# Optimization experiments

Measured on AMD Instinct MI355X. Metric: run time of the kernel, lower is better.

The kernel has to match this reference:

```python
import jax, jax.numpy as jnp
import numpy as np

D, NP, NC, ITERS = 2048, 64, 32, 3
B, L = 4, 4096
EPS = 1e-6


def setup_inputs() -> dict:
    key = jax.random.key(0)
    ks = jax.random.split(key, 10)
    sc = lambda k, shape, s: (jax.random.normal(k, shape, jnp.float32) * s)
    return {
        "x": jax.random.normal(ks[0], (B, L, D), jnp.float32),
        "prop_w": sc(ks[1], (NP, D), 0.02),
        "prop_b": jnp.zeros((NP,), jnp.float32),
        "constraint_mat": sc(ks[2], (NC, NP), 0.1),
        "polarity": sc(ks[3], (NC, NP), 0.1),
        "corr_w1": sc(ks[4], (2 * NP, 2 * NP), 0.08),
        "corr_b1": jnp.zeros((2 * NP,), jnp.float32),
        "corr_w2": sc(ks[5], (NP, 2 * NP), 0.08),
        "corr_b2": jnp.zeros((NP,), jnp.float32),
        "cons_w": sc(ks[6], (1, NC), 0.1),
        "cons_b": jnp.zeros((1,), jnp.float32),
        "emb_w": sc(ks[7], (D, NP), 0.02),
        "emb_b": jnp.zeros((D,), jnp.float32),
        "norm_w": jnp.ones((D,), jnp.float32),
    }


def reference(x, prop_w, prop_b, constraint_mat, polarity,
              corr_w1, corr_b1, corr_w2, corr_b2,
              cons_w, cons_b, emb_w, emb_b, norm_w):
    n_p = prop_w.shape[0]
    n_c = constraint_mat.shape[0]
    W = jax.nn.sigmoid(constraint_mat)  # [n_c, n_p] constraint strength
    P = jax.nn.sigmoid(polarity)        # [n_c, n_p] polarity

    def check(props):
        # mean_j(W_ij*p_j + P_ij*(1-p_j)) == (p @ W.T + (1-p) @ P.T) / n_p
        return (props @ W.T + (1.0 - props) @ P.T) / n_p  # [B,L,n_c]

    props = jax.nn.sigmoid(x @ prop_w.T + prop_b)  # [B,L,n_p]
    for _ in range(ITERS):
        violation = 1.0 - check(props)                 # [B,L,n_c]
        viol_signal = (violation @ W) / (n_c + 1e-06)  # [B,L,n_p]
        h = jnp.concatenate([props, viol_signal], axis=-1)  # [B,L,2*n_p]
        h = jax.nn.gelu(h @ corr_w1.T + corr_b1, approximate=False)
        props = jax.nn.sigmoid(h @ corr_w2.T + corr_b2)

    satisfaction = check(props)                              # [B,L,n_c]
    consistency = jax.nn.sigmoid(satisfaction @ cons_w.T + cons_b)  # [B,L,1]
    violation_loss = jnp.mean(1.0 - satisfaction)
    symbolic = props @ emb_w.T + emb_b                       # [B,L,D]
    y = x + symbolic * consistency
    y = y * jax.lax.rsqrt(jnp.mean(y * y, axis=-1, keepdims=True) + EPS) * norm_w
    return (y, props, satisfaction, consistency, violation_loss)
```

## Files before the change

### kernel.cpp

```cpp
#include <hip/hip_runtime.h>
#include <hip/hip_bf16.h>
#include <cstdint>

#define D     2048
#define NP    64
#define NC    32
#define T     16384

#define Y_OFF   0
#define P_OFF   33554432
#define S_OFF   34603008
#define C_OFF   35127296
#define L_OFF   35143680

#define WS_LPART 0
#define WS_SUMP  1024
#define WS_PWF   1056
#define WS_EF    66592
#define WS_W1F   132128
#define WS_W2F   140320
#define WS_WMF   144416
#define WS_WLF   145440

typedef short short8 __attribute__((ext_vector_type(8)));
typedef float f32x4 __attribute__((ext_vector_type(4)));

__device__ __forceinline__ float sigf(float z) { return 1.0f / (1.0f + __expf(-z)); }
__device__ __forceinline__ short f2bf(float f) {
  unsigned u = __float_as_uint(f);
  return (short)((u + 0x8000u) >> 16);
}
__device__ __forceinline__ unsigned pk2(float a, float b) {
  return ((unsigned)(unsigned short)f2bf(a)) | (((unsigned)(unsigned short)f2bf(b)) << 16);
}

__global__ __launch_bounds__(256) void k0_prep(const float* __restrict__ cm, const float* __restrict__ pol,
                                               const float* __restrict__ w1, const float* __restrict__ w2,
                                               const float* __restrict__ pw, const float* __restrict__ ew,
                                               float* __restrict__ ws) {
  int gid = blockIdx.x * 256 + threadIdx.x;
  int stride = gridDim.x * 256;
  short* pwF = (short*)(ws + WS_PWF);
  for (int idx = gid; idx < 64 * 4 * 64; idx += stride) {
    int kc = idx >> 8, jt = (idx >> 6) & 3, l = idx & 63;
    int j = 16 * jt + (l & 15), k = 32 * kc + 8 * (l >> 4);
    const float* src = &pw[(size_t)j * D + k];
    short8 v;
#pragma unroll
    for (int e = 0; e < 8; ++e) v[e] = f2bf(src[e]);
    *(short8*)&pwF[idx * 8] = v;
  }
  short* eF = (short*)(ws + WS_EF);
  for (int idx = gid; idx < 128 * 2 * 64; idx += stride) {
    int dt = idx >> 7, kc = (idx >> 6) & 1, l = idx & 63;
    int d = 16 * dt + (l & 15), j = 32 * kc + 8 * (l >> 4);
    const float* src = &ew[(size_t)d * NP + j];
    short8 v;
#pragma unroll
    for (int e = 0; e < 8; ++e) v[e] = f2bf(src[e]);
    *(short8*)&eF[idx * 8] = v;
  }
  short* w1F = (short*)(ws + WS_W1F);
  for (int idx = gid; idx < 8 * 4 * 64; idx += stride) {
    int nt = idx >> 8, kc = (idx >> 6) & 3, l = idx & 63;
    int m = 16 * nt + (l & 15), k = 32 * kc + 8 * (l >> 4);
    const float* src = &w1[(size_t)m * 128 + k];
    short8 v;
#pragma unroll
    for (int e = 0; e < 8; ++e) v[e] = f2bf(src[e]);
    *(short8*)&w1F[idx * 8] = v;
  }
  short* w2F = (short*)(ws + WS_W2F);
  for (int idx = gid; idx < 4 * 4 * 64; idx += stride) {
    int nt = idx >> 8, kc = (idx >> 6) & 3, l = idx & 63;
    int j = 16 * nt + (l & 15), k = 32 * kc + 8 * (l >> 4);
    const float* src = &w2[(size_t)j * 128 + k];
    short8 v;
#pragma unroll
    for (int e = 0; e < 8; ++e) v[e] = f2bf(src[e]);
    *(short8*)&w2F[idx * 8] = v;
  }
  short* wmF = (short*)(ws + WS_WMF);
  for (int idx = gid; idx < 2 * 2 * 64; idx += stride) {
    int nt = idx >> 7, kc = (idx >> 6) & 1, l = idx & 63;
    int i = 16 * nt + (l & 15), j = 32 * kc + 8 * (l >> 4);
    short8 v;
#pragma unroll
    for (int e = 0; e < 8; ++e)
      v[e] = f2bf(sigf(cm[i * 64 + j + e]) - sigf(pol[i * 64 + j + e]));
    *(short8*)&wmF[idx * 8] = v;
  }
  short* wlF = (short*)(ws + WS_WLF);
  for (int idx = gid; idx < 4 * 64; idx += stride) {
    int nt = idx >> 6, l = idx & 63;
    int j = 16 * nt + (l & 15), i0 = 8 * (l >> 4);
    short8 v;
#pragma unroll
    for (int e = 0; e < 8; ++e) v[e] = f2bf(sigf(cm[(i0 + e) * 64 + j]));
    *(short8*)&wlF[idx * 8] = v;
  }
  if (gid < NC) {
    float s = 0.f;
    for (int j = 0; j < NP; ++j) s += sigf(pol[gid * NP + j]);
    ws[WS_SUMP + gid] = s;
  }
}

__global__ __launch_bounds__(256) void k1_props(const float* __restrict__ x, const float* __restrict__ ws,
                                                const float* __restrict__ pb, float* __restrict__ props0) {
  __shared__ char XT[8192];
  int tid = threadIdx.x, lane = tid & 63;
  int jt = __builtin_amdgcn_readfirstlane(tid >> 6);
  int wv = tid >> 6;
  int t0 = blockIdx.x * 16;
  int lr = lane & 15, lg = lane >> 4;
  int c64 = tid & 63;
  const short* pwF = (const short*)(ws + WS_PWF);

  f32x4 acc = {0.f, 0.f, 0.f, 0.f};
  for (int c = 0; c < 8; ++c) {
    float4 st[4];
#pragma unroll
    for (int j = 0; j < 4; ++j)
      st[j] = *(const float4*)&x[(size_t)(t0 + wv + 4 * j) * D + 256 * c + 4 * c64];
    __syncthreads();
#pragma unroll
    for (int j = 0; j < 4; ++j) {
      int tt = wv + 4 * j;
      int off = (tt * 512 + 8 * c64) ^ ((tt & 7) << 4);
      uint2 p = make_uint2(pk2(st[j].x, st[j].y), pk2(st[j].z, st[j].w));
      *(uint2*)(XT + off) = p;
    }
    __syncthreads();
#pragma unroll
    for (int kcL = 0; kcL < 8; ++kcL) {
      const short8 b = *(const short8*)(XT + ((lr * 512 + 64 * kcL + 16 * lg) ^ ((lr & 7) << 4)));
      const short8 a = *(const short8*)&pwF[(((8 * c + kcL) * 4 + jt) * 64 + lane) * 8];
      acc = __builtin_amdgcn_mfma_f32_16x16x32_bf16(a, b, acc, 0, 0, 0);
    }
  }
  int j0 = 16 * jt + 4 * lg;
  const float4 pbv = *(const float4*)&pb[j0];
  float4 o;
  o.x = sigf(acc[0] + pbv.x); o.y = sigf(acc[1] + pbv.y);
  o.z = sigf(acc[2] + pbv.z); o.w = sigf(acc[3] + pbv.w);
  *(float4*)&props0[(size_t)(t0 + lr) * 64 + j0] = o;
}

__global__ __launch_bounds__(64) void k2_iter(const float* __restrict__ ws,
                                              const float* __restrict__ b1, const float* __restrict__ b2,
                                              const float* __restrict__ cw, const float* __restrict__ cb,
                                              const float* __restrict__ props0, float* __restrict__ out,
                                              float* __restrict__ lpart) {
  __shared__ char Lraw[9216];
  char* Hb = Lraw;
  char* H2b = Lraw + 4096;
  char* SBb = Lraw + 8192;
  int lane = threadIdx.x & 63;
  int lr = lane & 15, lg = lane >> 4;
  int t0 = blockIdx.x * 16;
  const short8* w1F = (const short8*)(ws + WS_W1F);
  const short8* w2F = (const short8*)(ws + WS_W2F);
  const short8* wmF = (const short8*)(ws + WS_WMF);
  const short8* wlF = (const short8*)(ws + WS_WLF);
  const float* SUMP = ws + WS_SUMP;

  float b1v[8], b2v[4], sumpv[2], cwv[2];
#pragma unroll
  for (int nt = 0; nt < 8; ++nt) b1v[nt] = b1[16 * nt + lr];
#pragma unroll
  for (int nt = 0; nt < 4; ++nt) b2v[nt] = b2[16 * nt + lr];
#pragma unroll
  for (int nt = 0; nt < 2; ++nt) { sumpv[nt] = SUMP[16 * nt + lr]; cwv[nt] = cw[16 * nt + lr]; }
  float cb0 = cb[0];

#pragma unroll
  for (int r = 0; r < 4; ++r) {
    int idx = r * 64 + lane;
    int t = idx >> 4, c4 = idx & 15;
    const float4 v = *(const float4*)&props0[(size_t)(t0 + t) * 64 + 4 * c4];
    int off = (t * 256 + c4 * 8) ^ ((t & 7) << 4);
    *(unsigned*)(Hb + off) = pk2(v.x, v.y);
    *(unsigned*)(Hb + off + 4) = pk2(v.z, v.w);
  }
  __syncthreads();

  const f32x4 zf = {0.f, 0.f, 0.f, 0.f};
  f32x4 s0, s1;

#define LDF(base, row, kelem, rowB) \
  (*(const short8*)((base) + ((((row) * (rowB)) + (kelem) * 2) ^ (((row) & 7) << 4))))
#define STBF(base, row, kelem, rowB, val) \
  (*(short*)((base) + ((((row) * (rowB)) + (kelem) * 2) ^ (((row) & 7) << 4))) = f2bf(val))

  for (int it = 0; it < 3; ++it) {
    short8 ap0 = LDF(Hb, lr, 8 * lg, 256);
    short8 ap1 = LDF(Hb, lr, 32 + 8 * lg, 256);
    s0 = zf; s1 = zf;
    s0 = __builtin_amdgcn_mfma_f32_16x16x32_bf16(ap0, wmF[0 * 64 + lane], s0, 0, 0, 0);
    s0 = __builtin_amdgcn_mfma_f32_16x16x32_bf16(ap1, wmF[1 * 64 + lane], s0, 0, 0, 0);
    s1 = __builtin_amdgcn_mfma_f32_16x16x32_bf16(ap0, wmF[2 * 64 + lane], s1, 0, 0, 0);
    s1 = __builtin_amdgcn_mfma_f32_16x16x32_bf16(ap1, wmF[3 * 64 + lane], s1, 0, 0, 0);
#pragma unroll
    for (int q = 0; q < 4; ++q) {
      int t = 4 * lg + q;
      STBF(SBb, t, lr, 64, 1.f - (s0[q] + sumpv[0]) * (1.f / 64.f));
      STBF(SBb, t, 16 + lr, 64, 1.f - (s1[q] + sumpv[1]) * (1.f / 64.f));
    }
    __syncthreads();

    short8 as = LDF(SBb, lr, 8 * lg, 64);
    f32x4 vv0 = __builtin_amdgcn_mfma_f32_16x16x32_bf16(as, wlF[0 * 64 + lane], zf, 0, 0, 0);
    f32x4 vv1 = __builtin_amdgcn_mfma_f32_16x16x32_bf16(as, wlF[1 * 64 + lane], zf, 0, 0, 0);
    f32x4 vv2 = __builtin_amdgcn_mfma_f32_16x16x32_bf16(as, wlF[2 * 64 + lane], zf, 0, 0, 0);
    f32x4 vv3 = __builtin_amdgcn_mfma_f32_16x16x32_bf16(as, wlF[3 * 64 + lane], zf, 0, 0, 0);
    const float vs = 1.0f / (32.0f + 1e-6f);
#pragma unroll
    for (int q = 0; q < 4; ++q) {
      int t = 4 * lg + q;
      STBF(Hb, t, 64 + lr, 256, vv0[q] * vs);
      STBF(Hb, t, 64 + 16 + lr, 256, vv1[q] * vs);
      STBF(Hb, t, 64 + 32 + lr, 256, vv2[q] * vs);
      STBF(Hb, t, 64 + 48 + lr, 256, vv3[q] * vs);
    }
    __syncthreads();

    short8 ah2 = LDF(Hb, lr, 64 + 8 * lg, 256);
    short8 ah3 = LDF(Hb, lr, 96 + 8 * lg, 256);
    f32x4 g1[8];
#pragma unroll
    for (int nt = 0; nt < 8; ++nt) {
      f32x4 a = zf;
      a = __builtin_amdgcn_mfma_f32_16x16x32_bf16(ap0, w1F[(nt * 4 + 0) * 64 + lane], a, 0, 0, 0);
      a = __builtin_amdgcn_mfma_f32_16x16x32_bf16(ap1, w1F[(nt * 4 + 1) * 64 + lane], a, 0, 0, 0);
      a = __builtin_amdgcn_mfma_f32_16x16x32_bf16(ah2, w1F[(nt * 4 + 2) * 64 + lane], a, 0, 0, 0);
      a = __builtin_amdgcn_mfma_f32_16x16x32_bf16(ah3, w1F[(nt * 4 + 3) * 64 + lane], a, 0, 0, 0);
      g1[nt] = a;
    }
#pragma unroll
    for (int nt = 0; nt < 8; ++nt) {
#pragma unroll
      for (int q = 0; q < 4; ++q) {
        float v = g1[nt][q] + b1v[nt];
        float gl = 0.5f * v * (1.0f + erff(v * 0.70710678118654752f));
        STBF(H2b, 4 * lg + q, 16 * nt + lr, 256, gl);
      }
    }
    __syncthreads();

    short8 ab0 = LDF(H2b, lr, 8 * lg, 256);
    short8 ab1 = LDF(H2b, lr, 32 + 8 * lg, 256);
    short8 ab2 = LDF(H2b, lr, 64 + 8 * lg, 256);
    short8 ab3 = LDF(H2b, lr, 96 + 8 * lg, 256);
#pragma unroll
    for (int nt = 0; nt < 4; ++nt) {
      f32x4 a = zf;
      a = __builtin_amdgcn_mfma_f32_16x16x32_bf16(ab0, w2F[(nt * 4 + 0) * 64 + lane], a, 0, 0, 0);
      a = __builtin_amdgcn_mfma_f32_16x16x32_bf16(ab1, w2F[(nt * 4 + 1) * 64 + lane], a, 0, 0, 0);
      a = __builtin_amdgcn_mfma_f32_16x16x32_bf16(ab2, w2F[(nt * 4 + 2) * 64 + lane], a, 0, 0, 0);
      a = __builtin_amdgcn_mfma_f32_16x16x32_bf16(ab3, w2F[(nt * 4 + 3) * 64 + lane], a, 0, 0, 0);
#pragma unroll
      for (int q = 0; q < 4; ++q) {
        int t = 4 * lg + q;
        float p = sigf(a[q] + b2v[nt]);
        STBF(Hb, t, 16 * nt + lr, 256, p);
        if (it == 2) out[P_OFF + (size_t)(t0 + t) * 64 + 16 * nt + lr] = p;
      }
    }
    __syncthreads();
  }

  {
    short8 ap0 = LDF(Hb, lr, 8 * lg, 256);
    short8 ap1 = LDF(Hb, lr, 32 + 8 * lg, 256);
    s0 = zf; s1 = zf;
    s0 = __builtin_amdgcn_mfma_f32_16x16x32_bf16(ap0, wmF[0 * 64 + lane], s0, 0, 0, 0);
    s0 = __builtin_amdgcn_mfma_f32_16x16x32_bf16(ap1, wmF[1 * 64 + lane], s0, 0, 0, 0);
    s1 = __builtin_amdgcn_mfma_f32_16x16x32_bf16(ap0, wmF[2 * 64 + lane], s1, 0, 0, 0);
    s1 = __builtin_amdgcn_mfma_f32_16x16x32_bf16(ap1, wmF[3 * 64 + lane], s1, 0, 0, 0);
    float ls = 0.f;
    float csum[4];
#pragma unroll
    for (int q = 0; q < 4; ++q) {
      int t = 4 * lg + q;
      float sa = (s0[q] + sumpv[0]) * (1.f / 64.f);
      float sb = (s1[q] + sumpv[1]) * (1.f / 64.f);
      out[S_OFF + (size_t)(t0 + t) * 32 + lr] = sa;
      out[S_OFF + (size_t)(t0 + t) * 32 + 16 + lr] = sb;
      ls += (1.f - sa) + (1.f - sb);
      csum[q] = cwv[0] * sa + cwv[1] * sb;
    }
#pragma unroll
    for (int m = 1; m <= 8; m <<= 1) {
#pragma unroll
      for (int q = 0; q < 4; ++q) csum[q] += __shfl_xor(csum[q], m);
    }
    if (lr == 0) {
#pragma unroll
      for (int q = 0; q < 4; ++q)
        out[C_OFF + t0 + 4 * lg + q] = sigf(csum[q] + cb0);
    }
#pragma unroll
    for (int m = 1; m <= 32; m <<= 1) ls += __shfl_xor(ls, m);
    if (lane == 0) lpart[blockIdx.x] = ls;
  }
#undef LDF
#undef STBF
}

__global__ __launch_bounds__(512) void k3n(const float* __restrict__ x, const float* __restrict__ ws,
                                           const float* __restrict__ eb, const float* __restrict__ nw,
                                           float* __restrict__ out) {
  __shared__ float ssp[8][16];
  __shared__ float sc16[16];
  int tid = threadIdx.x, lane = tid & 63;
  int wu = __builtin_amdgcn_readfirstlane(tid >> 6);
  int t0 = blockIdx.x * 16;
  int lr = lane & 15, lg = lane >> 4;
  const short* eF = (const short*)(ws + WS_EF);

  const float* pr = out + P_OFF + (size_t)(t0 + lr) * 64 + 8 * lg;
  const float4 q0 = *(const float4*)pr;
  const float4 q1 = *(const float4*)(pr + 4);
  const float4 q2 = *(const float4*)(pr + 32);
  const float4 q3 = *(const float4*)(pr + 36);
  short8 p0, p1;
  p0[0] = f2bf(q0.x); p0[1] = f2bf(q0.y); p0[2] = f2bf(q0.z); p0[3] = f2bf(q0.w);
  p0[4] = f2bf(q1.x); p0[5] = f2bf(q1.y); p0[6] = f2bf(q1.z); p0[7] = f2bf(q1.w);
  p1[0] = f2bf(q2.x); p1[1] = f2bf(q2.y); p1[2] = f2bf(q2.z); p1[3] = f2bf(q2.w);
  p1[4] = f2bf(q3.x); p1[5] = f2bf(q3.y); p1[6] = f2bf(q3.z); p1[7] = f2bf(q3.w);

  float consv = out[C_OFF + t0 + lr];

  f32x4 yv[16];
  float ss = 0.f;
#pragma unroll
  for (int dt2 = 0; dt2 < 16; ++dt2) {
    int dt = wu * 16 + dt2;
    const short8 e0 = *(const short8*)&eF[((dt * 2 + 0) * 64 + lane) * 8];
    const short8 e1 = *(const short8*)&eF[((dt * 2 + 1) * 64 + lane) * 8];
    f32x4 acc = {0.f, 0.f, 0.f, 0.f};
    acc = __builtin_amdgcn_mfma_f32_16x16x32_bf16(e0, p0, acc, 0, 0, 0);
    acc = __builtin_amdgcn_mfma_f32_16x16x32_bf16(e1, p1, acc, 0, 0, 0);
    int d0 = 16 * dt + 4 * lg;
    const float4 ebv = *(const float4*)&eb[d0];
    const float4 xv = *(const float4*)&x[(size_t)(t0 + lr) * D + d0];
    f32x4 y;
    y[0] = fmaf(acc[0] + ebv.x, consv, xv.x);
    y[1] = fmaf(acc[1] + ebv.y, consv, xv.y);
    y[2] = fmaf(acc[2] + ebv.z, consv, xv.z);
    y[3] = fmaf(acc[3] + ebv.w, consv, xv.w);
    ss += y[0] * y[0] + y[1] * y[1] + y[2] * y[2] + y[3] * y[3];
    yv[dt2] = y;
  }
  ss += __shfl_xor(ss, 16);
  ss += __shfl_xor(ss, 32);
  if (lg == 0) ssp[wu][lr] = ss;
  __syncthreads();
  if (tid < 16) {
    float s = 0.f;
#pragma unroll
    for (int w = 0; w < 8; ++w) s += ssp[w][tid];
    sc16[tid] = rsqrtf(s * (1.0f / 2048.0f) + 1e-6f);
  }
  __syncthreads();
  float sc = sc16[lr];
#pragma unroll
  for (int dt2 = 0; dt2 < 16; ++dt2) {
    int d0 = 16 * (wu * 16 + dt2) + 4 * lg;
    const float4 nwv = *(const float4*)&nw[d0];
    float4 o;
    o.x = yv[dt2][0] * sc * nwv.x;
    o.y = yv[dt2][1] * sc * nwv.y;
    o.z = yv[dt2][2] * sc * nwv.z;
    o.w = yv[dt2][3] * sc * nwv.w;
    *(float4*)&out[Y_OFF + (size_t)(t0 + lr) * D + d0] = o;
  }
}

__global__ __launch_bounds__(256) void k4_loss(const float* __restrict__ lpart, float* __restrict__ loss) {
  __shared__ float w[4];
  int tid = threadIdx.x;
  float v = 0.f;
#pragma unroll
  for (int r = 0; r < 4; ++r) v += lpart[tid + 256 * r];
  for (int o = 32; o > 0; o >>= 1) v += __shfl_down(v, o);
  if ((tid & 63) == 0) w[tid >> 6] = v;
  __syncthreads();
  if (tid == 0)
    loss[0] = (w[0] + w[1] + w[2] + w[3]) * (1.0f / (16384.0f * 32.0f));
}

extern "C" void kernel_launch(void* const* d_in, const int* in_sizes, int n_in,
                              void* d_out, int out_size, void* d_ws, size_t ws_size,
                              hipStream_t stream) {
  (void)in_sizes; (void)n_in; (void)out_size; (void)ws_size;
  const float* x   = (const float*)d_in[0];
  const float* pw  = (const float*)d_in[1];
  const float* pb  = (const float*)d_in[2];
  const float* cm  = (const float*)d_in[3];
  const float* pol = (const float*)d_in[4];
  const float* w1  = (const float*)d_in[5];
  const float* b1  = (const float*)d_in[6];
  const float* w2  = (const float*)d_in[7];
  const float* b2  = (const float*)d_in[8];
  const float* cw  = (const float*)d_in[9];
  const float* cb  = (const float*)d_in[10];
  const float* ew  = (const float*)d_in[11];
  const float* eb  = (const float*)d_in[12];
  const float* nw  = (const float*)d_in[13];
  float* out = (float*)d_out;
  float* ws  = (float*)d_ws;

  hipLaunchKernelGGL(k0_prep, dim3(64), dim3(256), 0, stream, cm, pol, w1, w2, pw, ew, ws);
  hipLaunchKernelGGL(k1_props, dim3(1024), dim3(256), 0, stream, x, ws, pb, out + Y_OFF);
  hipLaunchKernelGGL(k2_iter, dim3(1024), dim3(64), 0, stream, ws, b1, b2, cw, cb,
                     out + Y_OFF, out, ws + WS_LPART);
  hipLaunchKernelGGL(k4_loss, dim3(1), dim3(256), 0, stream, ws + WS_LPART, out + L_OFF);
  hipLaunchKernelGGL(k3n, dim3(1024), dim3(512), 0, stream, x, ws, eb, nw, out);
}
```

Baseline: 128.9 us.

## Fuse props projection with refinement, double-buffer x tiles, fold loss into norm

Merges the property projection and the iterative refinement into one kernel. The sigmoid props now go straight into LDS as bf16 instead of taking a global round trip, and one fewer launch is needed. The x tile load is double-buffered so global loads overlap the MFMA work. Inside the single-wave refinement, block barriers become LDS waitcnt fences. The separate loss-reduction kernel is folded into one wave of the final norm kernel. The norm kernel also holds y in bf16 registers to save VGPRs, which costs some output precision before the RMS scaling.

```diff
diff --git a/kernel.cpp b/kernel.cpp
--- a/kernel.cpp
+++ b/kernel.cpp
@@ -106,9 +106,15 @@
   }
 }
 
-__global__ __launch_bounds__(256) void k1_props(const float* __restrict__ x, const float* __restrict__ ws,
-                                                const float* __restrict__ pb, float* __restrict__ props0) {
-  __shared__ char XT[8192];
+__global__ __launch_bounds__(256, 4) void k12(const float* __restrict__ x, const float* __restrict__ ws,
+                                              const float* __restrict__ pb,
+                                              const float* __restrict__ b1, const float* __restrict__ b2,
+                                              const float* __restrict__ cw, const float* __restrict__ cb,
+                                              float* __restrict__ out, float* __restrict__ lpart) {
+  __shared__ __align__(16) char L[20480];
+  char* Hb = L;
+  char* H2b = L + 4096;
+  char* SBb = L + 8192;
   int tid = threadIdx.x, lane = tid & 63;
   int jt = __builtin_amdgcn_readfirstlane(tid >> 6);
   int wv = tid >> 6;
@@ -118,47 +124,54 @@
   const short* pwF = (const short*)(ws + WS_PWF);
 
   f32x4 acc = {0.f, 0.f, 0.f, 0.f};
-  for (int c = 0; c < 8; ++c) {
+  {
     float4 st[4];
 #pragma unroll
     for (int j = 0; j < 4; ++j)
-      st[j] = *(const float4*)&x[(size_t)(t0 + wv + 4 * j) * D + 256 * c + 4 * c64];
-    __syncthreads();
+      st[j] = *(const float4*)&x[(size_t)(t0 + wv + 4 * j) * D + 4 * c64];
+    char* XTw = L + 4096;
 #pragma unroll
     for (int j = 0; j < 4; ++j) {
       int tt = wv + 4 * j;
       int off = (tt * 512 + 8 * c64) ^ ((tt & 7) << 4);
-      uint2 p = make_uint2(pk2(st[j].x, st[j].y), pk2(st[j].z, st[j].w));
-      *(uint2*)(XT + off) = p;
-    }
-    __syncthreads();
-#pragma unroll
-    for (int kcL = 0; kcL < 8; ++kcL) {
-      const short8 b = *(const short8*)(XT + ((lr * 512 + 64 * kcL + 16 * lg) ^ ((lr & 7) << 4)));
-      const short8 a = *(const short8*)&pwF[(((8 * c + kcL) * 4 + jt) * 64 + lane) * 8];
-      acc = __builtin_amdgcn_mfma_f32_16x16x32_bf16(a, b, acc, 0, 0, 0);
-    }
-  }
-  int j0 = 16 * jt + 4 * lg;
-  const float4 pbv = *(const float4*)&pb[j0];
-  float4 o;
-  o.x = sigf(acc[0] + pbv.x); o.y = sigf(acc[1] + pbv.y);
-  o.z = sigf(acc[2] + pbv.z); o.w = sigf(acc[3] + pbv.w);
-  *(float4*)&props0[(size_t)(t0 + lr) * 64 + j0] = o;
-}
-
-__global__ __launch_bounds__(64) void k2_iter(const float* __restrict__ ws,
-                                              const float* __restrict__ b1, const float* __restrict__ b2,
-                                              const float* __restrict__ cw, const float* __restrict__ cb,
-                                              const float* __restrict__ props0, float* __restrict__ out,
-                                              float* __restrict__ lpart) {
-  __shared__ char Lraw[9216];
-  char* Hb = Lraw;
-  char* H2b = Lraw + 4096;
-  char* SBb = Lraw + 8192;
-  int lane = threadIdx.x & 63;
-  int lr = lane & 15, lg = lane >> 4;
-  int t0 = blockIdx.x * 16;
+      *(uint2*)(XTw + off) = make_uint2(pk2(st[j].x, st[j].y), pk2(st[j].z, st[j].w));
+    }
+    for (int c = 0; c < 8; ++c) {
+      if (c < 7) {
+#pragma unroll
+        for (int j = 0; j < 4; ++j)
+          st[j] = *(const float4*)&x[(size_t)(t0 + wv + 4 * j) * D + 256 * (c + 1) + 4 * c64];
+      }
+      __syncthreads();
+      const char* XTr = L + 4096 + (c & 1) * 8192;
+#pragma unroll
+      for (int kcL = 0; kcL < 8; ++kcL) {
+        const short8 b = *(const short8*)(XTr + ((lr * 512 + 64 * kcL + 16 * lg) ^ ((lr & 7) << 4)));
+        const short8 a = *(const short8*)&pwF[(((8 * c + kcL) * 4 + jt) * 64 + lane) * 8];
+        acc = __builtin_amdgcn_mfma_f32_16x16x32_bf16(a, b, acc, 0, 0, 0);
+      }
+      if (c < 7) {
+        char* XTn = L + 4096 + ((c + 1) & 1) * 8192;
+#pragma unroll
+        for (int j = 0; j < 4; ++j) {
+          int tt = wv + 4 * j;
+          int off = (tt * 512 + 8 * c64) ^ ((tt & 7) << 4);
+          *(uint2*)(XTn + off) = make_uint2(pk2(st[j].x, st[j].y), pk2(st[j].z, st[j].w));
+        }
+      }
+    }
+  }
+  {
+    int j0 = 16 * jt + 4 * lg;
+    const float4 pbv = *(const float4*)&pb[j0];
+    float p0 = sigf(acc[0] + pbv.x), p1 = sigf(acc[1] + pbv.y);
+    float p2 = sigf(acc[2] + pbv.z), p3 = sigf(acc[3] + pbv.w);
+    int off = (lr * 256 + j0 * 2) ^ ((lr & 7) << 4);
+    *(uint2*)(Hb + off) = make_uint2(pk2(p0, p1), pk2(p2, p3));
+  }
+  __syncthreads();
+  if (wv != 0) return;
+
   const short8* w1F = (const short8*)(ws + WS_W1F);
   const short8* w2F = (const short8*)(ws + WS_W2F);
   const short8* wmF = (const short8*)(ws + WS_WMF);
@@ -174,20 +187,10 @@
   for (int nt = 0; nt < 2; ++nt) { sumpv[nt] = SUMP[16 * nt + lr]; cwv[nt] = cw[16 * nt + lr]; }
   float cb0 = cb[0];
 
-#pragma unroll
-  for (int r = 0; r < 4; ++r) {
-    int idx = r * 64 + lane;
-    int t = idx >> 4, c4 = idx & 15;
-    const float4 v = *(const float4*)&props0[(size_t)(t0 + t) * 64 + 4 * c4];
-    int off = (t * 256 + c4 * 8) ^ ((t & 7) << 4);
-    *(unsigned*)(Hb + off) = pk2(v.x, v.y);
-    *(unsigned*)(Hb + off + 4) = pk2(v.z, v.w);
-  }
-  __syncthreads();
-
   const f32x4 zf = {0.f, 0.f, 0.f, 0.f};
   f32x4 s0, s1;
 
+#define LDSFENCE asm volatile("s_waitcnt lgkmcnt(0)" ::: "memory")
 #define LDF(base, row, kelem, rowB) \
   (*(const short8*)((base) + ((((row) * (rowB)) + (kelem) * 2) ^ (((row) & 7) << 4))))
 #define STBF(base, row, kelem, rowB, val) \
@@ -207,7 +210,7 @@
       STBF(SBb, t, lr, 64, 1.f - (s0[q] + sumpv[0]) * (1.f / 64.f));
       STBF(SBb, t, 16 + lr, 64, 1.f - (s1[q] + sumpv[1]) * (1.f / 64.f));
     }
-    __syncthreads();
+    LDSFENCE;
 
     short8 as = LDF(SBb, lr, 8 * lg, 64);
     f32x4 vv0 = __builtin_amdgcn_mfma_f32_16x16x32_bf16(as, wlF[0 * 64 + lane], zf, 0, 0, 0);
@@ -223,7 +226,7 @@
       STBF(Hb, t, 64 + 32 + lr, 256, vv2[q] * vs);
       STBF(Hb, t, 64 + 48 + lr, 256, vv3[q] * vs);
     }
-    __syncthreads();
+    LDSFENCE;
 
     short8 ah2 = LDF(Hb, lr, 64 + 8 * lg, 256);
     short8 ah3 = LDF(Hb, lr, 96 + 8 * lg, 256);
@@ -246,7 +249,7 @@
         STBF(H2b, 4 * lg + q, 16 * nt + lr, 256, gl);
       }
     }
-    __syncthreads();
+    LDSFENCE;
 
     short8 ab0 = LDF(H2b, lr, 8 * lg, 256);
     short8 ab1 = LDF(H2b, lr, 32 + 8 * lg, 256);
@@ -267,7 +270,7 @@
         if (it == 2) out[P_OFF + (size_t)(t0 + t) * 64 + 16 * nt + lr] = p;
       }
     }
-    __syncthreads();
+    LDSFENCE;
   }
 
   {
@@ -306,11 +309,12 @@
   }
 #undef LDF
 #undef STBF
-}
-
-__global__ __launch_bounds__(512) void k3n(const float* __restrict__ x, const float* __restrict__ ws,
-                                           const float* __restrict__ eb, const float* __restrict__ nw,
-                                           float* __restrict__ out) {
+#undef LDSFENCE
+}
+
+__global__ __launch_bounds__(512, 4) void k3n(const float* __restrict__ x, const float* __restrict__ ws,
+                                              const float* __restrict__ eb, const float* __restrict__ nw,
+                                              const float* __restrict__ lpart, float* __restrict__ out) {
   __shared__ float ssp[8][16];
   __shared__ float sc16[16];
   int tid = threadIdx.x, lane = tid & 63;
@@ -318,6 +322,15 @@
   int t0 = blockIdx.x * 16;
   int lr = lane & 15, lg = lane >> 4;
   const short* eF = (const short*)(ws + WS_EF);
+
+  if (blockIdx.x == 0 && wu == 7) {
+    float v = 0.f;
+#pragma unroll
+    for (int r = 0; r < 16; ++r) v += lpart[lane + 64 * r];
+#pragma unroll
+    for (int m = 1; m <= 32; m <<= 1) v += __shfl_xor(v, m);
+    if (lane == 0) out[L_OFF] = v * (1.0f / (16384.0f * 32.0f));
+  }
 
   const float* pr = out + P_OFF + (size_t)(t0 + lr) * 64 + 8 * lg;
   const float4 q0 = *(const float4*)pr;
@@ -332,9 +345,9 @@
 
   float consv = out[C_OFF + t0 + lr];
 
-  f32x4 yv[16];
+  uint2 yv[16];
   float ss = 0.f;
-#pragma unroll
+#pragma unroll 4
   for (int dt2 = 0; dt2 < 16; ++dt2) {
     int dt = wu * 16 + dt2;
     const short8 e0 = *(const short8*)&eF[((dt * 2 + 0) * 64 + lane) * 8];
@@ -345,13 +358,12 @@
     int d0 = 16 * dt + 4 * lg;
     const float4 ebv = *(const float4*)&eb[d0];
     const float4 xv = *(const float4*)&x[(size_t)(t0 + lr) * D + d0];
-    f32x4 y;
-    y[0] = fmaf(acc[0] + ebv.x, consv, xv.x);
-    y[1] = fmaf(acc[1] + ebv.y, consv, xv.y);
-    y[2] = fmaf(acc[2] + ebv.z, consv, xv.z);
-    y[3] = fmaf(acc[3] + ebv.w, consv, xv.w);
-    ss += y[0] * y[0] + y[1] * y[1] + y[2] * y[2] + y[3] * y[3];
-    yv[dt2] = y;
+    float y0 = fmaf(acc[0] + ebv.x, consv, xv.x);
+    float y1 = fmaf(acc[1] + ebv.y, consv, xv.y);
+    float y2 = fmaf(acc[2] + ebv.z, consv, xv.z);
+    float y3 = fmaf(acc[3] + ebv.w, consv, xv.w);
+    ss += y0 * y0 + y1 * y1 + y2 * y2 + y3 * y3;
+    yv[dt2] = make_uint2(pk2(y0, y1), pk2(y2, y3));
   }
   ss += __shfl_xor(ss, 16);
   ss += __shfl_xor(ss, 32);
@@ -365,30 +377,18 @@
   }
   __syncthreads();
   float sc = sc16[lr];
-#pragma unroll
+#pragma unroll 4
   for (int dt2 = 0; dt2 < 16; ++dt2) {
     int d0 = 16 * (wu * 16 + dt2) + 4 * lg;
     const float4 nwv = *(const float4*)&nw[d0];
+    uint2 p = yv[dt2];
     float4 o;
-    o.x = yv[dt2][0] * sc * nwv.x;
-    o.y = yv[dt2][1] * sc * nwv.y;
-    o.z = yv[dt2][2] * sc * nwv.z;
-    o.w = yv[dt2][3] * sc * nwv.w;
+    o.x = __uint_as_float(p.x << 16) * sc * nwv.x;
+    o.y = __uint_as_float(p.x & 0xffff0000u) * sc * nwv.y;
+    o.z = __uint_as_float(p.y << 16) * sc * nwv.z;
+    o.w = __uint_as_float(p.y & 0xffff0000u) * sc * nwv.w;
     *(float4*)&out[Y_OFF + (size_t)(t0 + lr) * D + d0] = o;
   }
-}
-
-__global__ __launch_bounds__(256) void k4_loss(const float* __restrict__ lpart, float* __restrict__ loss) {
-  __shared__ float w[4];
-  int tid = threadIdx.x;
-  float v = 0.f;
-#pragma unroll
-  for (int r = 0; r < 4; ++r) v += lpart[tid + 256 * r];
-  for (int o = 32; o > 0; o >>= 1) v += __shfl_down(v, o);
-  if ((tid & 63) == 0) w[tid >> 6] = v;
-  __syncthreads();
-  if (tid == 0)
-    loss[0] = (w[0] + w[1] + w[2] + w[3]) * (1.0f / (16384.0f * 32.0f));
 }
 
 extern "C" void kernel_launch(void* const* d_in, const int* in_sizes, int n_in,
@@ -412,10 +412,9 @@
   float* out = (float*)d_out;
   float* ws  = (float*)d_ws;
 
-  hipLaunchKernelGGL(k0_prep, dim3(64), dim3(256), 0, stream, cm, pol, w1, w2, pw, ew, ws);
-  hipLaunchKernelGGL(k1_props, dim3(1024), dim3(256), 0, stream, x, ws, pb, out + Y_OFF);
-  hipLaunchKernelGGL(k2_iter, dim3(1024), dim3(64), 0, stream, ws, b1, b2, cw, cb,
-                     out + Y_OFF, out, ws + WS_LPART);
-  hipLaunchKernelGGL(k4_loss, dim3(1), dim3(256), 0, stream, ws + WS_LPART, out + L_OFF);
-  hipLaunchKernelGGL(k3n, dim3(1024), dim3(512), 0, stream, x, ws, eb, nw, out);
-}
+  hipLaunchKernelGGL(k0_prep, dim3(128), dim3(256), 0, stream, cm, pol, w1, w2, pw, ew, ws);
+  hipLaunchKernelGGL(k12, dim3(1024), dim3(256), 0, stream, x, ws, pb, b1, b2, cw, cb,
+                     out, ws + WS_LPART);
+  hipLaunchKernelGGL(k3n, dim3(1024), dim3(512), 0, stream, x, ws, eb, nw,
+                     ws + WS_LPART, out);
+}
```

Result: slower. 229.0 us (+77.6%).
